# Kernel tuning notes

Hardware: AMD Instinct MI355X
Metric: run time of the kernel (lower is better)

Reference implementation:

```python
import jax, jax.numpy as jnp
import numpy as np

BATCH = 2048
N = 2 * BATCH
TEMP = 0.5
BN_EPS = 1e-5
COS_EPS = 1e-8

# Precompute (constant) flat indices of the negative entries: all (i,j) with
# j != i and j != i +- BATCH. Each row has exactly N-2 negatives.
_mask = np.ones((N, N), dtype=bool)
np.fill_diagonal(_mask, False)
for _i in range(BATCH):
    _mask[_i, BATCH + _i] = False
    _mask[BATCH + _i, _i] = False
NEG_IDX = np.nonzero(_mask.reshape(-1))[0]  # (N*(N-2),)


def _projector(h, W1, gamma, beta, W2, b2):
    # Linear (no bias) -> BatchNorm1d (training-mode batch stats) -> ReLU -> Linear
    x = h @ W1.T                                   # (B, latent)
    mu = jnp.mean(x, axis=0)
    var = jnp.mean(jnp.square(x - mu), axis=0)     # biased var, as torch BN
    x = (x - mu) * jax.lax.rsqrt(var + BN_EPS) * gamma + beta
    x = jax.nn.relu(x)
    return x @ W2.T + b2                           # (B, proj)


def setup_inputs() -> dict:
    key = jax.random.key(0)
    ks = jax.random.split(key, 4)
    latent, proj = 2048, 256
    return {
        "h_i": jax.random.normal(ks[0], (BATCH, latent), jnp.float32),
        "h_j": jax.random.normal(ks[1], (BATCH, latent), jnp.float32),
        "W1": jax.random.normal(ks[2], (latent, latent), jnp.float32) / np.sqrt(latent),
        "gamma": jnp.ones((latent,), jnp.float32),
        "beta": jnp.zeros((latent,), jnp.float32),
        "W2": jax.random.normal(ks[3], (proj, latent), jnp.float32) / np.sqrt(latent),
        "b2": jnp.zeros((proj,), jnp.float32),
    }


def reference(h_i, h_j, W1, gamma, beta, W2, b2):
    z_i = _projector(h_i, W1, gamma, beta, W2, b2)
    z_j = _projector(h_j, W1, gamma, beta, W2, b2)
    z = jnp.concatenate([z_i, z_j], axis=0)                      # (N, proj)
    # cosine similarity: normalize once, then a single GEMM
    zn = z / jnp.maximum(jnp.linalg.norm(z, axis=1, keepdims=True), COS_EPS)
    sim = (zn @ zn.T) / TEMP                                     # (N, N)
    sim_i_j = jnp.diagonal(sim, offset=BATCH)                    # (BATCH,)
    sim_j_i = jnp.diagonal(sim, offset=-BATCH)                   # (BATCH,)
    positives = jnp.concatenate([sim_i_j, sim_j_i])[:, None]     # (N, 1)
    negatives = sim.reshape(-1)[NEG_IDX].reshape(N, N - 2)       # (N, N-2)
    logits = jnp.concatenate([positives, negatives], axis=1)     # (N, N-1)
    # cross-entropy with label 0 for every row, reduction='sum', then / N
    loss = jnp.sum(jax.nn.logsumexp(logits, axis=1) - logits[:, 0]) / N
    return loss
```

## Files before the change

kernel.cpp:

```cpp
#include <hip/hip_runtime.h>
#include <math.h>

#define BATCH   2048
#define NROWS   4096
#define LATENT  2048
#define PROJ    256
#define TEMP_INV 2.0f
#define BN_EPS  1e-5f
#define COS_EPS 1e-8f

typedef __bf16 bf16x8 __attribute__((ext_vector_type(8)));
typedef float  f32x4  __attribute__((ext_vector_type(4)));

__device__ __forceinline__ unsigned short f2bf(float f) {
    union { float f; unsigned int u; } c; c.f = f;
    return (unsigned short)((c.u + 0x7FFFu + ((c.u >> 16) & 1u)) >> 16);
}
__device__ __forceinline__ float bf2f(unsigned short h) {
    union { unsigned int u; float f; } c; c.u = ((unsigned int)h) << 16;
    return c.f;
}

__device__ __forceinline__ void gl_lds16(const unsigned short* g, unsigned short* l) {
    __builtin_amdgcn_global_load_lds(
        (__attribute__((address_space(1))) void*)g,
        (__attribute__((address_space(3))) void*)l, 16, 0, 0);
}

#define G1 1048576
#define G2 2097152
#define G3 3145728
#define G4 3276800
__global__ __launch_bounds__(256) void cvt_all_kernel(
    const float* __restrict__ h_i, const float* __restrict__ h_j,
    const float* __restrict__ W1,  const float* __restrict__ W2,
    unsigned short* __restrict__ dst)
{
    int i = blockIdx.x * 256 + threadIdx.x;
    if (i >= G4) return;
    const float* src; int off;
    if (i < G1)      { src = h_i; off = i; }
    else if (i < G2) { src = h_j; off = i - G1; }
    else if (i < G3) { src = W1;  off = i - G2; }
    else             { src = W2;  off = i - G3; }
    float4 v = reinterpret_cast<const float4*>(src)[off];
    ushort4 o;
    o.x = f2bf(v.x); o.y = f2bf(v.y); o.z = f2bf(v.z); o.w = f2bf(v.w);
    reinterpret_cast<ushort4*>(dst)[i] = o;
}

template<int KSTRIDE, int KLEN, int WM, int WN>
__device__ __forceinline__ void mfma_loop(
    const unsigned short* __restrict__ Ab,
    const unsigned short* __restrict__ Bb,
    unsigned short* As, unsigned short* Bs,
    f32x4 acc[WM][WN], int tid)
{
    constexpr int BM = WM * 32;
    constexpr int BN = WN * 32;
    const int wid = tid >> 6, lane = tid & 63;
    const int mblk = (wid >> 1) * (WM * 16);
    const int nblk = (wid & 1) * (WN * 16);
    const int lr = lane & 15, lk = lane >> 4;
    for (int k0 = 0; k0 < KLEN; k0 += 32) {
        __syncthreads();
        #pragma unroll
        for (int u = 0; u < BM / 64; ++u) {
            int li = u * 256 + tid;
            gl_lds16(Ab + (size_t)(li >> 2) * KSTRIDE + k0 + (li & 3) * 8, As + li * 8);
        }
        #pragma unroll
        for (int u = 0; u < BN / 64; ++u) {
            int li = u * 256 + tid;
            gl_lds16(Bb + (size_t)(li >> 2) * KSTRIDE + k0 + (li & 3) * 8, Bs + li * 8);
        }
        __syncthreads();
        bf16x8 af[WM], bv[WN];
        #pragma unroll
        for (int i = 0; i < WM; ++i)
            af[i] = *reinterpret_cast<const bf16x8*>(As + (mblk + i * 16 + lr) * 32 + lk * 8);
        #pragma unroll
        for (int j = 0; j < WN; ++j)
            bv[j] = *reinterpret_cast<const bf16x8*>(Bs + (nblk + j * 16 + lr) * 32 + lk * 8);
        #pragma unroll
        for (int i = 0; i < WM; ++i)
            #pragma unroll
            for (int j = 0; j < WN; ++j)
                acc[i][j] = __builtin_amdgcn_mfma_f32_16x16x32_bf16(af[i], bv[j], acc[i][j], 0, 0, 0);
    }
}

__global__ __launch_bounds__(256) void gemm1_mfma(
    const unsigned short* __restrict__ Hb, const unsigned short* __restrict__ W1b,
    unsigned short* __restrict__ Xb, float* __restrict__ sums, float* __restrict__ sumsqs)
{
    __shared__ __align__(16) unsigned short As[64 * 32];
    __shared__ __align__(16) unsigned short Bs[128 * 32];
    const int tid = threadIdx.x;
    const int m0 = blockIdx.y * 64, n0 = blockIdx.x * 128;
    f32x4 zero = {0.f, 0.f, 0.f, 0.f};
    f32x4 acc[2][4];
    #pragma unroll
    for (int i = 0; i < 2; ++i)
        #pragma unroll
        for (int j = 0; j < 4; ++j) acc[i][j] = zero;
    mfma_loop<LATENT, LATENT, 2, 4>(Hb + (size_t)m0 * LATENT, W1b + (size_t)n0 * LATENT,
                                    As, Bs, acc, tid);
    const int wid = tid >> 6, lane = tid & 63;
    const int mblk = (wid >> 1) * 32, nblk = (wid & 1) * 64;
    const int lr = lane & 15, lq = lane >> 4;
    const int half = m0 >> 11;
    #pragma unroll
    for (int j = 0; j < 4; ++j) {
        float s = 0.f, q = 0.f;
        #pragma unroll
        for (int i = 0; i < 2; ++i)
            #pragma unroll
            for (int r = 0; r < 4; ++r) {
                float v = acc[i][j][r];
                s += v; q += v * v;
                int row = m0 + mblk + i * 16 + lq * 4 + r;
                int col = n0 + nblk + j * 16 + lr;
                Xb[(size_t)row * LATENT + col] = f2bf(v);
            }
        s += __shfl_xor(s, 16, 64);  q += __shfl_xor(q, 16, 64);
        s += __shfl_xor(s, 32, 64);  q += __shfl_xor(q, 32, 64);
        if (lq == 0) {
            int col = n0 + nblk + j * 16 + lr;
            atomicAdd(&sums[half * LATENT + col], s);
            atomicAdd(&sumsqs[half * LATENT + col], q);
        }
    }
}

__global__ __launch_bounds__(256) void bn_final_kernel(
    const float* __restrict__ sums, const float* __restrict__ sumsqs,
    const float* __restrict__ gamma, const float* __restrict__ beta,
    float* __restrict__ scaleA, float* __restrict__ shiftA)
{
    const int idx = blockIdx.x * 256 + threadIdx.x;
    const int c = idx & (LATENT - 1);
    float mu  = sums[idx] * (1.0f / BATCH);
    float var = sumsqs[idx] * (1.0f / BATCH) - mu * mu;
    float inv = rsqrtf(var + BN_EPS);
    float sc = gamma[c] * inv;
    scaleA[idx] = sc;
    shiftA[idx] = beta[c] - mu * sc;
}

__global__ __launch_bounds__(256) void bnrelu_kernel(
    unsigned short* __restrict__ Xb, const float* __restrict__ scaleA,
    const float* __restrict__ shiftA)
{
    int idx = (blockIdx.x * 256 + threadIdx.x) * 8;
    int row = idx >> 11;
    int col = idx & (LATENT - 1);
    int half = row >> 11;
    ushort4 a = *reinterpret_cast<const ushort4*>(Xb + idx);
    ushort4 b = *reinterpret_cast<const ushort4*>(Xb + idx + 4);
    float4 s0 = *reinterpret_cast<const float4*>(scaleA + half * LATENT + col);
    float4 s1 = *reinterpret_cast<const float4*>(scaleA + half * LATENT + col + 4);
    float4 h0 = *reinterpret_cast<const float4*>(shiftA + half * LATENT + col);
    float4 h1 = *reinterpret_cast<const float4*>(shiftA + half * LATENT + col + 4);
    ushort4 oa, ob;
    oa.x = f2bf(fmaxf(fmaf(bf2f(a.x), s0.x, h0.x), 0.f));
    oa.y = f2bf(fmaxf(fmaf(bf2f(a.y), s0.y, h0.y), 0.f));
    oa.z = f2bf(fmaxf(fmaf(bf2f(a.z), s0.z, h0.z), 0.f));
    oa.w = f2bf(fmaxf(fmaf(bf2f(a.w), s0.w, h0.w), 0.f));
    ob.x = f2bf(fmaxf(fmaf(bf2f(b.x), s1.x, h1.x), 0.f));
    ob.y = f2bf(fmaxf(fmaf(bf2f(b.y), s1.y, h1.y), 0.f));
    ob.z = f2bf(fmaxf(fmaf(bf2f(b.z), s1.z, h1.z), 0.f));
    ob.w = f2bf(fmaxf(fmaf(bf2f(b.w), s1.w, h1.w), 0.f));
    *reinterpret_cast<ushort4*>(Xb + idx) = oa;
    *reinterpret_cast<ushort4*>(Xb + idx + 4) = ob;
}

__global__ __launch_bounds__(256) void gemm2_mfma(
    const unsigned short* __restrict__ Xb, const unsigned short* __restrict__ W2b,
    float* __restrict__ Zp)
{
    __shared__ __align__(16) unsigned short As[128 * 32];
    __shared__ __align__(16) unsigned short Bs[64 * 32];
    const int tid = threadIdx.x;
    const int m0 = blockIdx.y * 128, n0 = blockIdx.x * 64, kc = blockIdx.z;
    f32x4 zero = {0.f, 0.f, 0.f, 0.f};
    f32x4 acc[4][2];
    #pragma unroll
    for (int i = 0; i < 4; ++i) { acc[i][0] = zero; acc[i][1] = zero; }
    mfma_loop<LATENT, 512, 4, 2>(Xb + (size_t)m0 * LATENT + kc * 512,
                                 W2b + (size_t)n0 * LATENT + kc * 512, As, Bs, acc, tid);
    float* Zk = Zp + (size_t)kc * NROWS * PROJ;
    const int wid = tid >> 6, lane = tid & 63;
    const int mblk = (wid >> 1) * 64, nblk = (wid & 1) * 32;
    const int lr = lane & 15, lq = lane >> 4;
    #pragma unroll
    for (int i = 0; i < 4; ++i)
        #pragma unroll
        for (int j = 0; j < 2; ++j)
            #pragma unroll
            for (int r = 0; r < 4; ++r) {
                int row = m0 + mblk + i * 16 + lq * 4 + r;
                int col = n0 + nblk + j * 16 + lr;
                Zk[(size_t)row * PROJ + col] = acc[i][j][r];
            }
}

__global__ __launch_bounds__(256) void rownorm_kernel(
    const float* __restrict__ Zp, const float* __restrict__ b2,
    unsigned short* __restrict__ ZNb)
{
    const int wave = threadIdx.x >> 6;
    const int lane = threadIdx.x & 63;
    const int row = blockIdx.x * 4 + wave;
    float v[4];
    float sq = 0.f;
    #pragma unroll
    for (int i = 0; i < 4; ++i) {
        int col = lane + i * 64;
        float t = b2[col];
        #pragma unroll
        for (int c = 0; c < 4; ++c)
            t += Zp[(size_t)c * NROWS * PROJ + (size_t)row * PROJ + col];
        v[i] = t;
        sq += t * t;
    }
    #pragma unroll
    for (int off = 32; off > 0; off >>= 1) sq += __shfl_xor(sq, off, 64);
    float inv = 1.0f / fmaxf(sqrtf(sq), COS_EPS);
    #pragma unroll
    for (int i = 0; i < 4; ++i)
        ZNb[(size_t)row * PROJ + lane + i * 64] = f2bf(v[i] * inv);
}

__global__ __launch_bounds__(256) void simlse_mfma(
    const unsigned short* __restrict__ ZNb, float* __restrict__ rowsum,
    float* __restrict__ dgA, float* __restrict__ posA)
{
    __shared__ __align__(16) unsigned short As[128 * 32];
    __shared__ __align__(16) unsigned short Bs[128 * 32];
    const int tid = threadIdx.x;
    const int r0 = blockIdx.y * 128, j0 = blockIdx.x * 128;
    f32x4 zero = {0.f, 0.f, 0.f, 0.f};
    f32x4 acc[4][4];
    #pragma unroll
    for (int i = 0; i < 4; ++i)
        #pragma unroll
        for (int j = 0; j < 4; ++j) acc[i][j] = zero;
    mfma_loop<PROJ, PROJ, 4, 4>(ZNb + (size_t)r0 * PROJ, ZNb + (size_t)j0 * PROJ,
                                As, Bs, acc, tid);
    const int wid = tid >> 6, lane = tid & 63;
    const int mblk = (wid >> 1) * 64, nblk = (wid & 1) * 64;
    const int lr = lane & 15, lq = lane >> 4;
    #pragma unroll
    for (int i = 0; i < 4; ++i)
        #pragma unroll
        for (int r = 0; r < 4; ++r) {
            int R = r0 + mblk + i * 16 + lq * 4 + r;
            int P = (R < BATCH) ? R + BATCH : R - BATCH;
            float t = 0.f;
            #pragma unroll
            for (int j = 0; j < 4; ++j) {
                int J = j0 + nblk + j * 16 + lr;
                float s = acc[i][j][r] * TEMP_INV;
                float e = __expf(s);
                t += e;
                if (J == R) dgA[R] = e;
                if (J == P) posA[R] = s;
            }
            t += __shfl_xor(t, 1, 64);
            t += __shfl_xor(t, 2, 64);
            t += __shfl_xor(t, 4, 64);
            t += __shfl_xor(t, 8, 64);
            if (lr == 0) atomicAdd(&rowsum[R], t);
        }
}

__global__ __launch_bounds__(256) void loss_kernel(
    const float* __restrict__ rowsum, const float* __restrict__ dgA,
    const float* __restrict__ posA, float* __restrict__ out)
{
    __shared__ float red[256];
    float s = 0.f;
    for (int r = threadIdx.x; r < NROWS; r += 256)
        s += logf(rowsum[r] - dgA[r]) - posA[r];
    red[threadIdx.x] = s;
    __syncthreads();
    for (int off = 128; off > 0; off >>= 1) {
        if (threadIdx.x < off) red[threadIdx.x] += red[threadIdx.x + off];
        __syncthreads();
    }
    if (threadIdx.x == 0) out[0] = red[0] * (1.0f / NROWS);
}

extern "C" void kernel_launch(void* const* d_in, const int* in_sizes, int n_in,
                              void* d_out, int out_size, void* d_ws, size_t ws_size,
                              hipStream_t stream)
{
    const float* h_i   = (const float*)d_in[0];
    const float* h_j   = (const float*)d_in[1];
    const float* W1    = (const float*)d_in[2];
    const float* gamma = (const float*)d_in[3];
    const float* beta  = (const float*)d_in[4];
    const float* W2    = (const float*)d_in[5];
    const float* b2    = (const float*)d_in[6];
    float* out = (float*)d_out;

    float* Zp     = (float*)d_ws;
    float* sums   = Zp + (size_t)4 * NROWS * PROJ;
    float* sumsqs = sums + 2 * LATENT;
    float* rowsum = sumsqs + 2 * LATENT;
    float* scaleA = rowsum + NROWS;
    float* shiftA = scaleA + 2 * LATENT;
    float* dgA    = shiftA + 2 * LATENT;
    float* posA   = dgA + NROWS;
    unsigned short* Hb  = (unsigned short*)(posA + NROWS);
    unsigned short* W1b = Hb + (size_t)NROWS * LATENT;
    unsigned short* W2b = W1b + (size_t)LATENT * LATENT;
    unsigned short* Xb  = W2b + (size_t)PROJ * LATENT;
    unsigned short* ZNb = Xb + (size_t)NROWS * LATENT;

    hipMemsetAsync(sums, 0, (size_t)(4 * LATENT + NROWS) * sizeof(float), stream);

    cvt_all_kernel<<<(G4 + 255) / 256, 256, 0, stream>>>(h_i, h_j, W1, W2, Hb);
    gemm1_mfma<<<dim3(LATENT / 128, NROWS / 64), 256, 0, stream>>>(Hb, W1b, Xb, sums, sumsqs);
    bn_final_kernel<<<(2 * LATENT) / 256, 256, 0, stream>>>(sums, sumsqs, gamma, beta, scaleA, shiftA);
    bnrelu_kernel<<<(NROWS * LATENT / 8) / 256, 256, 0, stream>>>(Xb, scaleA, shiftA);
    gemm2_mfma<<<dim3(PROJ / 64, NROWS / 128, 4), 256, 0, stream>>>(Xb, W2b, Zp);
    rownorm_kernel<<<NROWS / 4, 256, 0, stream>>>(Zp, b2, ZNb);
    simlse_mfma<<<dim3(NROWS / 128, NROWS / 128), 256, 0, stream>>>(ZNb, rowsum, dgA, posA);
    loss_kernel<<<1, 256, 0, stream>>>(rowsum, dgA, posA, out);
}
```

Baseline: 212.7 us.

## Swizzle LDS tiles in MFMA loop and fold BN finalize into BN-ReLU kernel

The shared MFMA loop now XOR-swizzles the 16-byte chunk position per row group, both when global_load_lds fills LDS and when fragments are read, so the 64-byte-stride row reads in the MFMA fragment loads hit fewer LDS bank conflicts. Separately, the small bn_final kernel is removed and each BN-ReLU thread recomputes mean, variance, scale and shift from the raw sums, dropping one launch and the scale/shift round trip at the cost of redundant rsqrt work per row. The swizzle changes which global addresses each thread fetches, so correctness depends on matching the write and read mappings.

```diff
diff --git a/kernel.cpp b/kernel.cpp
--- a/kernel.cpp
+++ b/kernel.cpp
@@ -25,6 +25,10 @@
     __builtin_amdgcn_global_load_lds(
         (__attribute__((address_space(1))) void*)g,
         (__attribute__((address_space(3))) void*)l, 16, 0, 0);
+}
+
+__device__ __forceinline__ int swz(int R, int lk) {
+    return R * 32 + ((lk ^ ((R >> 1) & 3)) << 3);
 }
 
 #define G1 1048576
@@ -67,21 +71,25 @@
         #pragma unroll
         for (int u = 0; u < BM / 64; ++u) {
             int li = u * 256 + tid;
-            gl_lds16(Ab + (size_t)(li >> 2) * KSTRIDE + k0 + (li & 3) * 8, As + li * 8);
+            int r = li >> 2;
+            int c = (li & 3) ^ ((li >> 3) & 3);
+            gl_lds16(Ab + (size_t)r * KSTRIDE + k0 + c * 8, As + li * 8);
         }
         #pragma unroll
         for (int u = 0; u < BN / 64; ++u) {
             int li = u * 256 + tid;
-            gl_lds16(Bb + (size_t)(li >> 2) * KSTRIDE + k0 + (li & 3) * 8, Bs + li * 8);
+            int r = li >> 2;
+            int c = (li & 3) ^ ((li >> 3) & 3);
+            gl_lds16(Bb + (size_t)r * KSTRIDE + k0 + c * 8, Bs + li * 8);
         }
         __syncthreads();
         bf16x8 af[WM], bv[WN];
         #pragma unroll
         for (int i = 0; i < WM; ++i)
-            af[i] = *reinterpret_cast<const bf16x8*>(As + (mblk + i * 16 + lr) * 32 + lk * 8);
+            af[i] = *reinterpret_cast<const bf16x8*>(As + swz(mblk + i * 16 + lr, lk));
         #pragma unroll
         for (int j = 0; j < WN; ++j)
-            bv[j] = *reinterpret_cast<const bf16x8*>(Bs + (nblk + j * 16 + lr) * 32 + lk * 8);
+            bv[j] = *reinterpret_cast<const bf16x8*>(Bs + swz(nblk + j * 16 + lr, lk));
         #pragma unroll
         for (int i = 0; i < WM; ++i)
             #pragma unroll
@@ -133,44 +141,39 @@
     }
 }
 
-__global__ __launch_bounds__(256) void bn_final_kernel(
-    const float* __restrict__ sums, const float* __restrict__ sumsqs,
-    const float* __restrict__ gamma, const float* __restrict__ beta,
-    float* __restrict__ scaleA, float* __restrict__ shiftA)
-{
-    const int idx = blockIdx.x * 256 + threadIdx.x;
-    const int c = idx & (LATENT - 1);
-    float mu  = sums[idx] * (1.0f / BATCH);
-    float var = sumsqs[idx] * (1.0f / BATCH) - mu * mu;
-    float inv = rsqrtf(var + BN_EPS);
-    float sc = gamma[c] * inv;
-    scaleA[idx] = sc;
-    shiftA[idx] = beta[c] - mu * sc;
-}
-
 __global__ __launch_bounds__(256) void bnrelu_kernel(
-    unsigned short* __restrict__ Xb, const float* __restrict__ scaleA,
-    const float* __restrict__ shiftA)
-{
-    int idx = (blockIdx.x * 256 + threadIdx.x) * 8;
-    int row = idx >> 11;
-    int col = idx & (LATENT - 1);
-    int half = row >> 11;
+    unsigned short* __restrict__ Xb, const float* __restrict__ sums,
+    const float* __restrict__ sumsqs, const float* __restrict__ gamma,
+    const float* __restrict__ beta)
+{
+    const int row = blockIdx.x;
+    const int half = row >> 11;
+    const int col = threadIdx.x * 8;
+    size_t idx = (size_t)row * LATENT + col;
     ushort4 a = *reinterpret_cast<const ushort4*>(Xb + idx);
     ushort4 b = *reinterpret_cast<const ushort4*>(Xb + idx + 4);
-    float4 s0 = *reinterpret_cast<const float4*>(scaleA + half * LATENT + col);
-    float4 s1 = *reinterpret_cast<const float4*>(scaleA + half * LATENT + col + 4);
-    float4 h0 = *reinterpret_cast<const float4*>(shiftA + half * LATENT + col);
-    float4 h1 = *reinterpret_cast<const float4*>(shiftA + half * LATENT + col + 4);
+    const float* S = sums + half * LATENT + col;
+    const float* Q = sumsqs + half * LATENT + col;
+    float4 s0 = *reinterpret_cast<const float4*>(S);
+    float4 s1 = *reinterpret_cast<const float4*>(S + 4);
+    float4 q0 = *reinterpret_cast<const float4*>(Q);
+    float4 q1 = *reinterpret_cast<const float4*>(Q + 4);
+    float4 g0 = *reinterpret_cast<const float4*>(gamma + col);
+    float4 g1 = *reinterpret_cast<const float4*>(gamma + col + 4);
+    float4 e0 = *reinterpret_cast<const float4*>(beta + col);
+    float4 e1 = *reinterpret_cast<const float4*>(beta + col + 4);
     ushort4 oa, ob;
-    oa.x = f2bf(fmaxf(fmaf(bf2f(a.x), s0.x, h0.x), 0.f));
-    oa.y = f2bf(fmaxf(fmaf(bf2f(a.y), s0.y, h0.y), 0.f));
-    oa.z = f2bf(fmaxf(fmaf(bf2f(a.z), s0.z, h0.z), 0.f));
-    oa.w = f2bf(fmaxf(fmaf(bf2f(a.w), s0.w, h0.w), 0.f));
-    ob.x = f2bf(fmaxf(fmaf(bf2f(b.x), s1.x, h1.x), 0.f));
-    ob.y = f2bf(fmaxf(fmaf(bf2f(b.y), s1.y, h1.y), 0.f));
-    ob.z = f2bf(fmaxf(fmaf(bf2f(b.z), s1.z, h1.z), 0.f));
-    ob.w = f2bf(fmaxf(fmaf(bf2f(b.w), s1.w, h1.w), 0.f));
+    #define BN1(x, sv, qv, gv, ev, o) { \
+        float mu = (sv) * (1.0f / BATCH); \
+        float var = (qv) * (1.0f / BATCH) - mu * mu; \
+        float sc = (gv) * rsqrtf(var + BN_EPS); \
+        float sh = (ev) - mu * sc; \
+        o = f2bf(fmaxf(fmaf(bf2f(x), sc, sh), 0.f)); }
+    BN1(a.x, s0.x, q0.x, g0.x, e0.x, oa.x) BN1(a.y, s0.y, q0.y, g0.y, e0.y, oa.y)
+    BN1(a.z, s0.z, q0.z, g0.z, e0.z, oa.z) BN1(a.w, s0.w, q0.w, g0.w, e0.w, oa.w)
+    BN1(b.x, s1.x, q1.x, g1.x, e1.x, ob.x) BN1(b.y, s1.y, q1.y, g1.y, e1.y, ob.y)
+    BN1(b.z, s1.z, q1.z, g1.z, e1.z, ob.z) BN1(b.w, s1.w, q1.w, g1.w, e1.w, ob.w)
+    #undef BN1
     *reinterpret_cast<ushort4*>(Xb + idx) = oa;
     *reinterpret_cast<ushort4*>(Xb + idx + 4) = ob;
 }
@@ -309,9 +312,7 @@
     float* sums   = Zp + (size_t)4 * NROWS * PROJ;
     float* sumsqs = sums + 2 * LATENT;
     float* rowsum = sumsqs + 2 * LATENT;
-    float* scaleA = rowsum + NROWS;
-    float* shiftA = scaleA + 2 * LATENT;
-    float* dgA    = shiftA + 2 * LATENT;
+    float* dgA    = rowsum + NROWS;
     float* posA   = dgA + NROWS;
     unsigned short* Hb  = (unsigned short*)(posA + NROWS);
     unsigned short* W1b = Hb + (size_t)NROWS * LATENT;
@@ -323,8 +324,7 @@
 
     cvt_all_kernel<<<(G4 + 255) / 256, 256, 0, stream>>>(h_i, h_j, W1, W2, Hb);
     gemm1_mfma<<<dim3(LATENT / 128, NROWS / 64), 256, 0, stream>>>(Hb, W1b, Xb, sums, sumsqs);
-    bn_final_kernel<<<(2 * LATENT) / 256, 256, 0, stream>>>(sums, sumsqs, gamma, beta, scaleA, shiftA);
-    bnrelu_kernel<<<(NROWS * LATENT / 8) / 256, 256, 0, stream>>>(Xb, scaleA, shiftA);
+    bnrelu_kernel<<<NROWS, 256, 0, stream>>>(Xb, sums, sumsqs, gamma, beta);
     gemm2_mfma<<<dim3(PROJ / 64, NROWS / 128, 4), 256, 0, stream>>>(Xb, W2b, Zp);
     rownorm_kernel<<<NROWS / 4, 256, 0, stream>>>(Zp, b2, ZNb);
     simlse_mfma<<<dim3(NROWS / 128, NROWS / 128), 256, 0, stream>>>(ZNb, rowsum, dgA, posA);
```

Measured after the change: 213.2 us. Within noise of the previous version (+0.2%).
